# Kernel optimization log

Hardware: AMD Instinct MI355X
Metric: run time of the kernel (lower is better)

## Reference

```python
import jax, jax.numpy as jnp
import numpy as np

NDIM = 1024
NHEAD = 16
B, T = 4, 2048
EPS = 1e-05
GELU_C = np.sqrt(2.0 / np.pi).astype(np.float32)


def new_gelu(x):
    return 0.5 * x * (1.0 + jnp.tanh(GELU_C * (x + 0.044715 * x ** 3)))


def layer_norm(x, w, b):
    mu = jnp.mean(x, axis=-1, keepdims=True)
    var = jnp.var(x, axis=-1, keepdims=True)
    return (x - mu) * jax.lax.rsqrt(var + EPS) * w + b


def setup_inputs() -> dict:
    key = jax.random.key(0)
    ks = jax.random.split(key, 8)
    d, dff = NDIM, 4 * NDIM
    s = 0.02
    return {
        "x": jax.random.normal(ks[0], (B, T, d), jnp.float32),
        "ln1_w": jnp.ones((d,), jnp.float32),
        "ln1_b": jnp.zeros((d,), jnp.float32),
        "w_attn": jax.random.normal(ks[1], (d, 3 * d), jnp.float32) * s,
        "b_attn": jnp.zeros((3 * d,), jnp.float32),
        "w_proj": jax.random.normal(ks[2], (d, d), jnp.float32) * s,
        "b_proj": jnp.zeros((d,), jnp.float32),
        "ln2_w": jnp.ones((d,), jnp.float32),
        "ln2_b": jnp.zeros((d,), jnp.float32),
        "w_fc": jax.random.normal(ks[3], (d, dff), jnp.float32) * s,
        "b_fc": jnp.zeros((dff,), jnp.float32),
        "w_fc2": jax.random.normal(ks[4], (dff, d), jnp.float32) * s,
        "b_fc2": jnp.zeros((d,), jnp.float32),
    }


def reference(x, ln1_w, ln1_b, w_attn, b_attn, w_proj, b_proj,
              ln2_w, ln2_b, w_fc, b_fc, w_fc2, b_fc2):
    Bx, Tx, C = x.shape
    hd = C // NHEAD
    # --- attention ---
    h = layer_norm(x, ln1_w, ln1_b)
    qkv = h @ w_attn + b_attn                       # [B,T,3C]
    q, k, v = jnp.split(qkv, 3, axis=-1)
    q = q.reshape(Bx, Tx, NHEAD, hd).transpose(0, 2, 1, 3)  # [B,H,T,hd]
    k = k.reshape(Bx, Tx, NHEAD, hd).transpose(0, 2, 1, 3)
    v = v.reshape(Bx, Tx, NHEAD, hd).transpose(0, 2, 1, 3)
    att = jnp.einsum('bhqd,bhkd->bhqk', q, k) * (1.0 / np.sqrt(hd).astype(np.float32))
    causal = jnp.tril(jnp.ones((Tx, Tx), bool))
    att = jnp.where(causal[None, None], att, jnp.float32(-jnp.inf))
    att = jax.nn.softmax(att, axis=-1)
    y = jnp.einsum('bhqk,bhkd->bhqd', att, v)
    y = y.transpose(0, 2, 1, 3).reshape(Bx, Tx, C)
    x = x + y @ w_proj + b_proj
    # --- MLP ---
    h2 = layer_norm(x, ln2_w, ln2_b)
    x = x + new_gelu(h2 @ w_fc + b_fc) @ w_fc2 + b_fc2
    return x
```

## Files before the change

### kernel.cpp

```cpp
#include <hip/hip_runtime.h>

typedef __attribute__((ext_vector_type(8))) short short8;
typedef __attribute__((ext_vector_type(8))) unsigned short ushort8;
typedef __attribute__((ext_vector_type(4))) float f32x4;
typedef __attribute__((ext_vector_type(16))) float f32x16;
typedef __attribute__((ext_vector_type(2))) unsigned int uint2v;
typedef unsigned int uint32;

__device__ __forceinline__ unsigned short f2bf(float f){
  union { float f; unsigned int u; } x; x.f = f;
  unsigned int u = x.u;
  u += 0x7fffu + ((u >> 16) & 1u);
  return (unsigned short)(u >> 16);
}
__device__ __forceinline__ float bf2f(unsigned short s){
  union { float f; unsigned int u; } x; x.u = ((uint32)s) << 16; return x.f;
}

typedef __attribute__((address_space(1))) void gvoid;
typedef __attribute__((address_space(3))) void lvoid;
__device__ __forceinline__ void gload_lds16(const void* g, void* l){
  __builtin_amdgcn_global_load_lds((gvoid*)g, (lvoid*)l, 16, 0, 0);
}

__device__ __forceinline__ f32x4 mfma_bf16(short8 a, short8 b, f32x4 c){
  return __builtin_amdgcn_mfma_f32_16x16x32_bf16(a, b, c, 0, 0, 0);
}
__device__ __forceinline__ f32x16 mfma32(short8 a, short8 b, f32x16 c){
  return __builtin_amdgcn_mfma_f32_32x32x16_bf16(a, b, c, 0, 0, 0);
}

__device__ __forceinline__ uint32 cvtpk_bf(float lo, float hi){
  uint32 r;
  asm("v_cvt_pk_bf16_f32 %0, %1, %2" : "=v"(r) : "v"(lo), "v"(hi));
  return r;
}
__device__ __forceinline__ void plswap(uint32& a, uint32& b){
  auto r = __builtin_amdgcn_permlane32_swap(a, b, false, false);
  a = r[0]; b = r[1];
}

#if __has_builtin(__builtin_amdgcn_exp2f)
__device__ __forceinline__ float exp2g(float x){ return __builtin_amdgcn_exp2f(x); }
#else
__device__ __forceinline__ float exp2g(float x){ return exp2f(x); }
#endif
#if __has_builtin(__builtin_amdgcn_rcpf)
__device__ __forceinline__ float rcpg(float x){ return __builtin_amdgcn_rcpf(x); }
#else
__device__ __forceinline__ float rcpg(float x){ return 1.0f / x; }
#endif

__device__ __forceinline__ float gelu_fast(float v){
  const float u = 0.7978845608028654f * (v + 0.044715f * v * v * v);
  const float E = exp2g(2.8853900817779268f * u);
  return v - v * rcpg(1.0f + E);
}

__device__ __forceinline__ f32x16 zero16(){
  f32x16 z;
  #pragma unroll
  for (int i = 0; i < 16; i++) z[i] = 0.0f;
  return z;
}

__global__ __launch_bounds__(256) void wtrans_kernel(
    const float* __restrict__ w, unsigned short* __restrict__ wt, int K, int N)
{
  __shared__ float tile[32][33];
  const int n0 = blockIdx.x * 32;
  const int k0 = blockIdx.y * 32;
  const int t = threadIdx.x;
  #pragma unroll
  for (int i = 0; i < 4; i++){
    const int e = t + i * 256;
    const int r = e >> 5, c = e & 31;
    tile[r][c] = w[(size_t)(k0 + r) * N + n0 + c];
  }
  __syncthreads();
  #pragma unroll
  for (int i = 0; i < 4; i++){
    const int e = t + i * 256;
    const int r = e >> 5, c = e & 31;
    wt[(size_t)(n0 + r) * K + k0 + c] = f2bf(tile[c][r]);
  }
}

__global__ __launch_bounds__(256) void vtrans_kernel(
    const unsigned short* __restrict__ qkv, unsigned short* __restrict__ vt)
{
  __shared__ unsigned short tile[32][33];
  const int bh = blockIdx.z;
  const int b = bh >> 4, h = bh & 15;
  const int t0 = blockIdx.x * 32;
  const int f0 = blockIdx.y * 32;
  const int t = threadIdx.x;
  #pragma unroll
  for (int i = 0; i < 4; i++){
    const int e = t + i * 256;
    const int r = e >> 5, c = e & 31;
    tile[r][c] = qkv[(size_t)(b * 2048 + t0 + r) * 3072 + 2048 + h * 64 + f0 + c];
  }
  __syncthreads();
  #pragma unroll
  for (int i = 0; i < 4; i++){
    const int e = t + i * 256;
    const int r = e >> 5, c = e & 31;
    vt[((size_t)bh * 64 + f0 + r) * 2048 + t0 + c] = tile[c][r];
  }
}

__global__ __launch_bounds__(256) void ln_kernel(
    const float* __restrict__ x, const float* __restrict__ w, const float* __restrict__ b,
    unsigned short* __restrict__ out)
{
  const int row = blockIdx.x;
  const int t = threadIdx.x;
  const float4 v = ((const float4*)(x + (size_t)row * 1024))[t];
  float s  = v.x + v.y + v.z + v.w;
  float s2 = v.x * v.x + v.y * v.y + v.z * v.z + v.w * v.w;
  #pragma unroll
  for (int off = 32; off > 0; off >>= 1){
    s  += __shfl_xor(s, off);
    s2 += __shfl_xor(s2, off);
  }
  __shared__ float ps[8];
  const int wid = t >> 6;
  if ((t & 63) == 0){ ps[wid] = s; ps[4 + wid] = s2; }
  __syncthreads();
  s  = ps[0] + ps[1] + ps[2] + ps[3];
  s2 = ps[4] + ps[5] + ps[6] + ps[7];
  const float mu  = s * (1.0f / 1024.0f);
  const float var = s2 * (1.0f / 1024.0f) - mu * mu;
  const float rs  = rsqrtf(var + 1e-5f);
  const float4 wv = ((const float4*)w)[t];
  const float4 bv = ((const float4*)b)[t];
  ushort4 ov;
  ov.x = f2bf((v.x - mu) * rs * wv.x + bv.x);
  ov.y = f2bf((v.y - mu) * rs * wv.y + bv.y);
  ov.z = f2bf((v.z - mu) * rs * wv.z + bv.z);
  ov.w = f2bf((v.w - mu) * rs * wv.w + bv.w);
  ((ushort4*)(out + (size_t)row * 1024))[t] = ov;
}

#define EPI_BF16   0
#define EPI_RESF32 1
#define EPI_GELU   2

template<int EPI>
__global__ __launch_bounds__(256, 2) void gemm5_kernel(
    const unsigned short* __restrict__ A,
    const unsigned short* __restrict__ BT,
    const float* __restrict__ bias,
    const float* __restrict__ res,
    void* __restrict__ outp,
    int M, int N, int K)
{
  constexpr int SLOT = 24576;
  __shared__ __align__(16) char lds[3 * SLOT];

  const int nwg = gridDim.x;
  const int bid = blockIdx.x;
  const int wg = (bid & 7) * (nwg >> 3) + (bid >> 3);
  const int NT = N >> 8;
  const int mt = wg / NT;
  const int nti = wg - mt * NT;
  const int m0 = mt << 7;
  const int n0 = nti << 8;

  const int tid = threadIdx.x;
  const int lane = tid & 63;
  const int wid = tid >> 6;
  const int fr = lane & 15;
  const int fg = lane >> 4;

  const unsigned short* aSrc[2]; int aDst[2];
  #pragma unroll
  for (int l = 0; l < 2; l++){
    const int s = l * 256 + tid;
    const int r = s >> 2, c = s & 3;
    aSrc[l] = A + (size_t)(m0 + r) * K + ((c ^ ((r >> 1) & 3)) << 3);
    aDst[l] = s * 16;
  }
  const unsigned short* bSrc[4]; int bDst[4];
  #pragma unroll
  for (int l = 0; l < 4; l++){
    const int s = l * 256 + tid;
    const int r = s >> 2, c = s & 3;
    bSrc[l] = BT + (size_t)(n0 + r) * K + ((c ^ ((r >> 1) & 3)) << 3);
    bDst[l] = 8192 + s * 16;
  }

  int aOff[8], bOff[4];
  #pragma unroll
  for (int mi = 0; mi < 8; mi++){
    const int row = mi * 16 + fr;
    aOff[mi] = row * 64 + ((fg ^ ((row >> 1) & 3)) << 4);
  }
  #pragma unroll
  for (int nj = 0; nj < 4; nj++){
    const int row = wid * 64 + nj * 16 + fr;
    bOff[nj] = 8192 + row * 64 + ((fg ^ ((row >> 1) & 3)) << 4);
  }

  f32x4 acc[8][4];
  #pragma unroll
  for (int i = 0; i < 8; i++)
    #pragma unroll
    for (int j = 0; j < 4; j++) acc[i][j] = (f32x4){0.f, 0.f, 0.f, 0.f};

#define STAGE5(sl, slot) do { \
    gload_lds16(aSrc[0] + (size_t)(sl) * 32, lds + (slot) + aDst[0]); \
    gload_lds16(aSrc[1] + (size_t)(sl) * 32, lds + (slot) + aDst[1]); \
    gload_lds16(bSrc[0] + (size_t)(sl) * 32, lds + (slot) + bDst[0]); \
    gload_lds16(bSrc[1] + (size_t)(sl) * 32, lds + (slot) + bDst[1]); \
    gload_lds16(bSrc[2] + (size_t)(sl) * 32, lds + (slot) + bDst[2]); \
    gload_lds16(bSrc[3] + (size_t)(sl) * 32, lds + (slot) + bDst[3]); \
  } while (0)

  const int NS = K >> 5;

  STAGE5(0, 0);
  STAGE5(1, SLOT);
  asm volatile("s_waitcnt vmcnt(6)" ::: "memory");
  __builtin_amdgcn_s_barrier();
  asm volatile("" ::: "memory");

  int cs = 0, cg = 2 * SLOT;
  for (int s = 0; s < NS; s++){
    short8 aF[8], bF[4];
    #pragma unroll
    for (int mi = 0; mi < 8; mi++)
      aF[mi] = *(const short8*)(lds + cs + aOff[mi]);
    #pragma unroll
    for (int nj = 0; nj < 4; nj++)
      bF[nj] = *(const short8*)(lds + cs + bOff[nj]);
    if (s + 2 < NS) STAGE5(s + 2, cg);
    #pragma unroll
    for (int mi = 0; mi < 8; mi++)
      #pragma unroll
      for (int nj = 0; nj < 4; nj++)
        acc[mi][nj] = mfma_bf16(aF[mi], bF[nj], acc[mi][nj]);

    if (s + 2 < NS){
      asm volatile("s_waitcnt vmcnt(6)" ::: "memory");
    } else if (s + 1 < NS){
      asm volatile("s_waitcnt vmcnt(0)" ::: "memory");
    }
    __builtin_amdgcn_s_barrier();
    asm volatile("" ::: "memory");

    cs += SLOT; if (cs == 3 * SLOT) cs = 0;
    cg += SLOT; if (cg == 3 * SLOT) cg = 0;
  }
#undef STAGE5

  #pragma unroll
  for (int mi = 0; mi < 8; mi++){
    const int mrow = m0 + mi * 16 + fg * 4;
    #pragma unroll
    for (int nj = 0; nj < 4; nj++){
      const int ncol = n0 + wid * 64 + nj * 16 + fr;
      const float bv = bias[ncol];
      #pragma unroll
      for (int r2 = 0; r2 < 4; r2++){
        const size_t idx = (size_t)(mrow + r2) * N + ncol;
        float v = acc[mi][nj][r2] + bv;
        if (EPI == EPI_RESF32){
          ((float*)outp)[idx] = v + res[idx];
        } else if (EPI == EPI_GELU){
          ((unsigned short*)outp)[idx] = f2bf(gelu_fast(v));
        } else {
          ((unsigned short*)outp)[idx] = f2bf(v);
        }
      }
    }
  }
}

template<int EPI, int BN>
__global__ __launch_bounds__(512, 2) void gemm4_kernel(
    const unsigned short* __restrict__ A,
    const unsigned short* __restrict__ BT,
    const float* __restrict__ bias,
    const float* __restrict__ res,
    void* __restrict__ outp,
    int M, int N, int K)
{
  constexpr int MI   = (BN == 256) ? 8 : 4;
  constexpr int SP   = MI / 4;
  constexpr int NBL  = BN / 128;
  constexpr int WN   = (BN == 256) ? 4 : 2;
  constexpr int WROWS= (BN == 256) ? 128 : 64;
  constexpr int ASL  = 16384;
  constexpr int SLOT = ASL + BN * 64;
  __shared__ __align__(16) char lds[4 * SLOT];

  const int nwg = gridDim.x;
  const int bid = blockIdx.x;
  const int wg = (bid & 7) * (nwg >> 3) + (bid >> 3);
  const int NTile = N / BN;
  const int mt = wg / NTile;
  const int nti = wg - mt * NTile;
  const int m0 = mt << 8;
  const int n0 = nti * BN;

  const int tid = threadIdx.x;
  const int lane = tid & 63;
  const int wid = tid >> 6;
  const int wv_m = wid / WN;
  const int wv_n = wid % WN;
  const int fr = lane & 15;
  const int fg = lane >> 4;

  const unsigned short* aSrc[2];
  int aDst[2];
  #pragma unroll
  for (int l = 0; l < 2; l++){
    const int s = l * 512 + tid;
    const int r = s >> 2, c = s & 3;
    aSrc[l] = A + (size_t)(m0 + r) * K + ((c ^ ((r >> 1) & 3)) << 3);
    aDst[l] = s * 16;
  }
  const unsigned short* bSrc[NBL];
  int bDst[NBL];
  #pragma unroll
  for (int l = 0; l < NBL; l++){
    const int s = l * 512 + tid;
    const int r = s >> 2, c = s & 3;
    bSrc[l] = BT + (size_t)(n0 + r) * K + ((c ^ ((r >> 1) & 3)) << 3);
    bDst[l] = ASL + s * 16;
  }

  int aOff[MI], bOff[4];
  #pragma unroll
  for (int mi = 0; mi < MI; mi++){
    const int row = wv_m * WROWS + mi * 16 + fr;
    aOff[mi] = row * 64 + ((fg ^ ((row >> 1) & 3)) << 4);
  }
  #pragma unroll
  for (int nj = 0; nj < 4; nj++){
    const int row = wv_n * 64 + nj * 16 + fr;
    bOff[nj] = ASL + row * 64 + ((fg ^ ((row >> 1) & 3)) << 4);
  }

  f32x4 acc[MI][4];
  #pragma unroll
  for (int i = 0; i < MI; i++)
    #pragma unroll
    for (int j = 0; j < 4; j++) acc[i][j] = (f32x4){0.f, 0.f, 0.f, 0.f};

#define STAGE_A(sl, slot) do { \
    gload_lds16(aSrc[0] + (size_t)(sl) * 32, lds + (slot) + aDst[0]); \
    gload_lds16(aSrc[1] + (size_t)(sl) * 32, lds + (slot) + aDst[1]); \
  } while (0)
#define STAGE_B(sl, slot) do { \
    gload_lds16(bSrc[0] + (size_t)(sl) * 32, lds + (slot) + bDst[0]); \
    if (NBL == 2) gload_lds16(bSrc[1] + (size_t)(sl) * 32, lds + (slot) + bDst[1]); \
  } while (0)

  const int NS = K >> 5;

  STAGE_A(0, 0);        STAGE_B(0, 0);
  STAGE_A(1, SLOT);     STAGE_B(1, SLOT);
  STAGE_A(2, 2 * SLOT); STAGE_B(2, 2 * SLOT);
  if (BN == 256) asm volatile("s_waitcnt vmcnt(8)" ::: "memory");
  else           asm volatile("s_waitcnt vmcnt(6)" ::: "memory");
  __builtin_amdgcn_s_barrier();

  for (int s = 0; s < NS; s++){
    const int ss = (s & 3) * SLOT;
    const int sg = ((s + 3) & 3) * SLOT;
    const bool pf = (s + 3 < NS);
    short8 bF[4];
    #pragma unroll
    for (int sp = 0; sp < SP; sp++){
      short8 aF[4];
      #pragma unroll
      for (int i = 0; i < 4; i++)
        aF[i] = *(const short8*)(lds + ss + aOff[sp * 4 + i]);
      if (sp == 0){
        #pragma unroll
        for (int nj = 0; nj < 4; nj++)
          bF[nj] = *(const short8*)(lds + ss + bOff[nj]);
      }
      if (pf){
        if (SP == 2){
          if (sp == 0) STAGE_A(s + 3, sg);
          else         STAGE_B(s + 3, sg);
        } else {
          STAGE_A(s + 3, sg);
          STAGE_B(s + 3, sg);
        }
      }
      __builtin_amdgcn_s_barrier();
      asm volatile("s_waitcnt lgkmcnt(0)" ::: "memory");
      __builtin_amdgcn_sched_barrier(0);
      __builtin_amdgcn_s_setprio(1);
      #pragma unroll
      for (int i = 0; i < 4; i++)
        #pragma unroll
        for (int nj = 0; nj < 4; nj++)
          acc[sp * 4 + i][nj] = mfma_bf16(aF[i], bF[nj], acc[sp * 4 + i][nj]);
      __builtin_amdgcn_s_setprio(0);
      if (sp == SP - 1){
        if (s + 3 < NS){
          if (BN == 256) asm volatile("s_waitcnt vmcnt(8)" ::: "memory");
          else           asm volatile("s_waitcnt vmcnt(6)" ::: "memory");
        } else if (s + 2 < NS){
          if (BN == 256) asm volatile("s_waitcnt vmcnt(4)" ::: "memory");
          else           asm volatile("s_waitcnt vmcnt(3)" ::: "memory");
        } else if (s + 1 < NS){
          asm volatile("s_waitcnt vmcnt(0)" ::: "memory");
        }
      }
      __builtin_amdgcn_s_barrier();
    }
  }
#undef STAGE_A
#undef STAGE_B

  #pragma unroll
  for (int mi = 0; mi < MI; mi++){
    const int mrow = m0 + wv_m * WROWS + mi * 16 + fg * 4;
    #pragma unroll
    for (int nj = 0; nj < 4; nj++){
      const int ncol = n0 + wv_n * 64 + nj * 16 + fr;
      const float bv = bias[ncol];
      #pragma unroll
      for (int r2 = 0; r2 < 4; r2++){
        const size_t idx = (size_t)(mrow + r2) * N + ncol;
        float v = acc[mi][nj][r2] + bv;
        if (EPI == EPI_RESF32){
          ((float*)outp)[idx] = v + res[idx];
        } else if (EPI == EPI_GELU){
          ((unsigned short*)outp)[idx] = f2bf(gelu_fast(v));
        } else {
          ((unsigned short*)outp)[idx] = f2bf(v);
        }
      }
    }
  }
}

template<bool MASK>
__device__ __forceinline__ void attn_tile(
    const unsigned short* __restrict__ Kc, const unsigned short* __restrict__ Vc,
    const short8 (&qf)[4], int kvbase, int qg, int l31, int hi,
    float& m_r, float& lsum, f32x16& Oa, f32x16& Ob)
{
  f32x16 Sa = zero16();
  f32x16 Sb = zero16();
  const int xb = l31 & 7;
  #pragma unroll
  for (int kk = 0; kk < 4; kk++){
    const int x = kk * 2 + hi;
    const short8 k0 = *(const short8*)((const char*)Kc + l31 * 128 + ((x ^ xb) << 4));
    const short8 k1 = *(const short8*)((const char*)Kc + (l31 + 32) * 128 + ((x ^ xb) << 4));
    Sa = mfma32(k0, qf[kk], Sa);
    Sb = mfma32(k1, qf[kk], Sb);
  }
  if (MASK){
    #pragma unroll
    for (int r = 0; r < 16; r++){
      const int kva = kvbase + (r & 3) + 8 * (r >> 2) + 4 * hi;
      Sa[r] = (kva > qg)      ? -1e30f : Sa[r];
      Sb[r] = (kva + 32 > qg) ? -1e30f : Sb[r];
    }
  }
  float tmax = Sa[0];
  #pragma unroll
  for (int r = 1; r < 16; r++) tmax = fmaxf(tmax, Sa[r]);
  #pragma unroll
  for (int r = 0; r < 16; r++) tmax = fmaxf(tmax, Sb[r]);
  tmax = fmaxf(tmax, __shfl_xor(tmax, 32));
  if (__any(tmax > m_r + 10.0f)){
    const float mn = fmaxf(m_r, tmax);
    const float sc = exp2g(m_r - mn);
    m_r = mn;
    lsum *= sc;
    #pragma unroll
    for (int r = 0; r < 16; r++){ Oa[r] *= sc; Ob[r] *= sc; }
  }
  float rs = 0.0f;
  #pragma unroll
  for (int r = 0; r < 16; r++){
    Sa[r] = exp2g(Sa[r] - m_r); rs += Sa[r];
    Sb[r] = exp2g(Sb[r] - m_r); rs += Sb[r];
  }
  rs += __shfl_xor(rs, 32);
  lsum += rs;

  short8 pf[4];
  {
    uint32 a0 = cvtpk_bf(Sa[0], Sa[1]),   b0 = cvtpk_bf(Sa[4], Sa[5]);
    uint32 a1 = cvtpk_bf(Sa[2], Sa[3]),   b1 = cvtpk_bf(Sa[6], Sa[7]);
    plswap(a0, b0); plswap(a1, b1);
    uint32 a2 = cvtpk_bf(Sa[8], Sa[9]),   b2 = cvtpk_bf(Sa[12], Sa[13]);
    uint32 a3 = cvtpk_bf(Sa[10], Sa[11]), b3 = cvtpk_bf(Sa[14], Sa[15]);
    plswap(a2, b2); plswap(a3, b3);
    union { uint32 u[4]; short8 s; } m0, m1;
    m0.u[0] = a0; m0.u[1] = a1; m0.u[2] = b0; m0.u[3] = b1;
    m1.u[0] = a2; m1.u[1] = a3; m1.u[2] = b2; m1.u[3] = b3;
    pf[0] = m0.s; pf[1] = m1.s;
  }
  {
    uint32 a0 = cvtpk_bf(Sb[0], Sb[1]),   b0 = cvtpk_bf(Sb[4], Sb[5]);
    uint32 a1 = cvtpk_bf(Sb[2], Sb[3]),   b1 = cvtpk_bf(Sb[6], Sb[7]);
    plswap(a0, b0); plswap(a1, b1);
    uint32 a2 = cvtpk_bf(Sb[8], Sb[9]),   b2 = cvtpk_bf(Sb[12], Sb[13]);
    uint32 a3 = cvtpk_bf(Sb[10], Sb[11]), b3 = cvtpk_bf(Sb[14], Sb[15]);
    plswap(a2, b2); plswap(a3, b3);
    union { uint32 u[4]; short8 s; } m0, m1;
    m0.u[0] = a0; m0.u[1] = a1; m0.u[2] = b0; m0.u[3] = b1;
    m1.u[0] = a2; m1.u[1] = a3; m1.u[2] = b2; m1.u[3] = b3;
    pf[2] = m0.s; pf[3] = m1.s;
  }
  #pragma unroll
  for (int kk = 0; kk < 4; kk++){
    const int x = kk * 2 + hi;
    const short8 v0 = *(const short8*)((const char*)Vc + l31 * 128 + ((x ^ xb) << 4));
    const short8 v1 = *(const short8*)((const char*)Vc + (l31 + 32) * 128 + ((x ^ xb) << 4));
    Oa = mfma32(v0, pf[kk], Oa);
    Ob = mfma32(v1, pf[kk], Ob);
  }
}

__global__ __launch_bounds__(256) void attn_kernel(
    const unsigned short* __restrict__ qkv,
    const unsigned short* __restrict__ vt,
    unsigned short* __restrict__ y)
{
  __shared__ __align__(16) unsigned short Klds[2][4096];
  __shared__ __align__(16) unsigned short Vlds[2][4096];
  const int bid = blockIdx.x;
  const int bh = bid & 63;
  const int qb_i = bid >> 6;
  const int b = bh >> 4, h = bh & 15;
  const int qb0 = qb_i * 128;
  const int tid = threadIdx.x;
  const int w = tid >> 6;
  const int lane = tid & 63;
  const int l31 = lane & 31;
  const int hi = lane >> 5;

  const int qrow_g = b * 2048 + qb0 + w * 32 + l31;
  const unsigned short* qp = qkv + (size_t)qrow_g * 3072 + h * 64;
  short8 qf[4];
  #pragma unroll
  for (int kk = 0; kk < 4; kk++){
    short8 raw = *(const short8*)&qp[kk * 16 + hi * 8];
    #pragma unroll
    for (int j = 0; j < 8; j++)
      qf[kk][j] = (short)f2bf(bf2f((unsigned short)raw[j]) * 0.18033688011112042f);
  }

  const int sr = tid >> 3;
  const int ce = ((tid & 7) ^ (sr & 7)) * 8;
  const unsigned short* kb = qkv + (size_t)(b * 2048) * 3072 + 1024 + h * 64;
  const unsigned short* vb = vt + (size_t)bh * 64 * 2048;

  f32x16 Oa = zero16(), Ob = zero16();
  float m_r = -1e30f, lsum = 0.0f;
  const int qmin = qb0 + w * 32;
  const int qmax = qmin + 31;
  const int qg = qmin + l31;
  const int nkv = (qb0 >> 6) + 2;

#define STAGE(t, bb) do { \
    const size_t kro = (size_t)((t) * 64 + sr) * 3072; \
    gload_lds16(kb + kro + ce,                         (char*)&Klds[bb][0] + tid * 16); \
    gload_lds16(kb + kro + (size_t)32 * 3072 + ce,     (char*)&Klds[bb][0] + 4096 + tid * 16); \
    gload_lds16(vb + (size_t)sr * 2048 + (t) * 64 + ce,        (char*)&Vlds[bb][0] + tid * 16); \
    gload_lds16(vb + (size_t)(sr + 32) * 2048 + (t) * 64 + ce, (char*)&Vlds[bb][0] + 4096 + tid * 16); \
  } while (0)

  STAGE(0, 0);
  __syncthreads();
  int cur = 0;
  for (int kvt = 0; kvt < nkv; kvt++){
    if (kvt + 1 < nkv){
      if (cur) STAGE(kvt + 1, 0); else STAGE(kvt + 1, 1);
    }
    if (kvt * 64 <= qmax){
      if (kvt * 64 + 63 <= qmin)
        attn_tile<false>(Klds[cur], Vlds[cur], qf, kvt * 64, qg, l31, hi, m_r, lsum, Oa, Ob);
      else
        attn_tile<true >(Klds[cur], Vlds[cur], qf, kvt * 64, qg, l31, hi, m_r, lsum, Oa, Ob);
    }
    __syncthreads();
    cur ^= 1;
  }
#undef STAGE

  const float inv = 1.0f / lsum;
  unsigned short* yp = y + (size_t)qrow_g * 1024 + h * 64;
  #pragma unroll
  for (int c2 = 0; c2 < 4; c2++){
    uint2v da, db;
    da.x = cvtpk_bf(Oa[4 * c2 + 0] * inv, Oa[4 * c2 + 1] * inv);
    da.y = cvtpk_bf(Oa[4 * c2 + 2] * inv, Oa[4 * c2 + 3] * inv);
    *(uint2v*)&yp[8 * c2 + 4 * hi] = da;
    db.x = cvtpk_bf(Ob[4 * c2 + 0] * inv, Ob[4 * c2 + 1] * inv);
    db.y = cvtpk_bf(Ob[4 * c2 + 2] * inv, Ob[4 * c2 + 3] * inv);
    *(uint2v*)&yp[32 + 8 * c2 + 4 * hi] = db;
  }
}

extern "C" void kernel_launch(void* const* d_in, const int* in_sizes, int n_in,
                              void* d_out, int out_size, void* d_ws, size_t ws_size,
                              hipStream_t stream)
{
  const float* x      = (const float*)d_in[0];
  const float* ln1_w  = (const float*)d_in[1];
  const float* ln1_b  = (const float*)d_in[2];
  const float* w_attn = (const float*)d_in[3];
  const float* b_attn = (const float*)d_in[4];
  const float* w_proj = (const float*)d_in[5];
  const float* b_proj = (const float*)d_in[6];
  const float* ln2_w  = (const float*)d_in[7];
  const float* ln2_b  = (const float*)d_in[8];
  const float* w_fc   = (const float*)d_in[9];
  const float* b_fc   = (const float*)d_in[10];
  const float* w_fc2  = (const float*)d_in[11];
  const float* b_fc2  = (const float*)d_in[12];

  char* ws = (char*)d_ws;
  unsigned short* wbT_attn = (unsigned short*)(ws + 0);
  unsigned short* wbT_proj = (unsigned short*)(ws + 6291456);
  unsigned short* wbT_fc   = (unsigned short*)(ws + 8388608);
  unsigned short* wbT_fc2  = (unsigned short*)(ws + 16777216);
  unsigned short* h_bf     = (unsigned short*)(ws + 25165824);
  unsigned short* qkv_bf   = (unsigned short*)(ws + 41943040);
  unsigned short* vt_bf    = (unsigned short*)(ws + 92274688);
  unsigned short* g_bf     = (unsigned short*)(ws + 41943040);
  unsigned short* y_bf     = (unsigned short*)(ws + 109051904);
  float*          x1       = (float*)(ws + 125829120);
  float* outf = (float*)d_out;

  wtrans_kernel<<<dim3(3072/32, 1024/32), 256, 0, stream>>>(w_attn, wbT_attn, 1024, 3072);
  wtrans_kernel<<<dim3(1024/32, 1024/32), 256, 0, stream>>>(w_proj, wbT_proj, 1024, 1024);
  wtrans_kernel<<<dim3(4096/32, 1024/32), 256, 0, stream>>>(w_fc,   wbT_fc,   1024, 4096);
  wtrans_kernel<<<dim3(1024/32, 4096/32), 256, 0, stream>>>(w_fc2,  wbT_fc2,  4096, 1024);

  ln_kernel<<<8192, 256, 0, stream>>>(x, ln1_w, ln1_b, h_bf);
  gemm5_kernel<EPI_BF16><<<768, 256, 0, stream>>>(
      h_bf, wbT_attn, b_attn, nullptr, qkv_bf, 8192, 3072, 1024);
  vtrans_kernel<<<dim3(64, 2, 64), 256, 0, stream>>>(qkv_bf, vt_bf);
  attn_kernel<<<1024, 256, 0, stream>>>(qkv_bf, vt_bf, y_bf);
  gemm4_kernel<EPI_RESF32, 128><<<256, 512, 0, stream>>>(
      y_bf, wbT_proj, b_proj, x, x1, 8192, 1024, 1024);
  ln_kernel<<<8192, 256, 0, stream>>>(x1, ln2_w, ln2_b, h_bf);
  gemm5_kernel<EPI_GELU><<<1024, 256, 0, stream>>>(
      h_bf, wbT_fc, b_fc, nullptr, g_bf, 8192, 4096, 1024);
  gemm4_kernel<EPI_RESF32, 128><<<256, 512, 0, stream>>>(
      g_bf, wbT_fc2, b_fc2, x1, outf, 8192, 1024, 4096);
}
```

Measured before the change: 359.3 us.

## Replace N=1024 GEMMs with 64x256-tile, 2-wave kernel using 3-slot pipeline

Swaps the 512-thread 256x128-tile GEMM used for the attention projection and FC2 for a new 128-thread kernel with 64x256 tiles. Each of the two waves covers 64 rows by 128 columns, and the kernel uses a 3-slot LDS ring with prefetch distance 2 and one barrier per K step. The intent is to launch 512 smaller blocks so the 256 CUs are better filled, and to reduce barrier and sub-phase overhead. In exchange each block gets less A-operand reuse and fewer waves to hide latency, and the setprio and scheduling barriers are dropped.

```diff
diff --git a/kernel.cpp b/kernel.cpp
--- a/kernel.cpp
+++ b/kernel.cpp
@@ -278,8 +278,8 @@
   }
 }
 
-template<int EPI, int BN>
-__global__ __launch_bounds__(512, 2) void gemm4_kernel(
+template<int EPI>
+__global__ __launch_bounds__(128, 2) void gemm6_kernel(
     const unsigned short* __restrict__ A,
     const unsigned short* __restrict__ BT,
     const float* __restrict__ bias,
@@ -287,145 +287,115 @@
     void* __restrict__ outp,
     int M, int N, int K)
 {
-  constexpr int MI   = (BN == 256) ? 8 : 4;
-  constexpr int SP   = MI / 4;
-  constexpr int NBL  = BN / 128;
-  constexpr int WN   = (BN == 256) ? 4 : 2;
-  constexpr int WROWS= (BN == 256) ? 128 : 64;
-  constexpr int ASL  = 16384;
-  constexpr int SLOT = ASL + BN * 64;
-  __shared__ __align__(16) char lds[4 * SLOT];
+  constexpr int SLOT = 20480;
+  __shared__ __align__(16) char lds[3 * SLOT];
 
   const int nwg = gridDim.x;
   const int bid = blockIdx.x;
   const int wg = (bid & 7) * (nwg >> 3) + (bid >> 3);
-  const int NTile = N / BN;
-  const int mt = wg / NTile;
-  const int nti = wg - mt * NTile;
-  const int m0 = mt << 8;
-  const int n0 = nti * BN;
+  const int NT = N >> 8;
+  const int mt = wg / NT;
+  const int nti = wg - mt * NT;
+  const int m0 = mt << 6;
+  const int n0 = nti << 8;
 
   const int tid = threadIdx.x;
   const int lane = tid & 63;
   const int wid = tid >> 6;
-  const int wv_m = wid / WN;
-  const int wv_n = wid % WN;
   const int fr = lane & 15;
   const int fg = lane >> 4;
 
-  const unsigned short* aSrc[2];
-  int aDst[2];
+  const unsigned short* aSrc[2]; int aDst[2];
   #pragma unroll
   for (int l = 0; l < 2; l++){
-    const int s = l * 512 + tid;
+    const int s = l * 128 + tid;
     const int r = s >> 2, c = s & 3;
     aSrc[l] = A + (size_t)(m0 + r) * K + ((c ^ ((r >> 1) & 3)) << 3);
     aDst[l] = s * 16;
   }
-  const unsigned short* bSrc[NBL];
-  int bDst[NBL];
-  #pragma unroll
-  for (int l = 0; l < NBL; l++){
-    const int s = l * 512 + tid;
+  const unsigned short* bSrc[8]; int bDst[8];
+  #pragma unroll
+  for (int l = 0; l < 8; l++){
+    const int s = l * 128 + tid;
     const int r = s >> 2, c = s & 3;
     bSrc[l] = BT + (size_t)(n0 + r) * K + ((c ^ ((r >> 1) & 3)) << 3);
-    bDst[l] = ASL + s * 16;
-  }
-
-  int aOff[MI], bOff[4];
-  #pragma unroll
-  for (int mi = 0; mi < MI; mi++){
-    const int row = wv_m * WROWS + mi * 16 + fr;
+    bDst[l] = 4096 + s * 16;
+  }
+
+  int aOff[4], bOff[8];
+  #pragma unroll
+  for (int mi = 0; mi < 4; mi++){
+    const int row = mi * 16 + fr;
     aOff[mi] = row * 64 + ((fg ^ ((row >> 1) & 3)) << 4);
   }
   #pragma unroll
-  for (int nj = 0; nj < 4; nj++){
-    const int row = wv_n * 64 + nj * 16 + fr;
-    bOff[nj] = ASL + row * 64 + ((fg ^ ((row >> 1) & 3)) << 4);
-  }
-
-  f32x4 acc[MI][4];
-  #pragma unroll
-  for (int i = 0; i < MI; i++)
-    #pragma unroll
-    for (int j = 0; j < 4; j++) acc[i][j] = (f32x4){0.f, 0.f, 0.f, 0.f};
-
-#define STAGE_A(sl, slot) do { \
+  for (int nj = 0; nj < 8; nj++){
+    const int row = wid * 128 + nj * 16 + fr;
+    bOff[nj] = 4096 + row * 64 + ((fg ^ ((row >> 1) & 3)) << 4);
+  }
+
+  f32x4 acc[4][8];
+  #pragma unroll
+  for (int i = 0; i < 4; i++)
+    #pragma unroll
+    for (int j = 0; j < 8; j++) acc[i][j] = (f32x4){0.f, 0.f, 0.f, 0.f};
+
+#define STAGE6(sl, slot) do { \
     gload_lds16(aSrc[0] + (size_t)(sl) * 32, lds + (slot) + aDst[0]); \
     gload_lds16(aSrc[1] + (size_t)(sl) * 32, lds + (slot) + aDst[1]); \
+    gload_lds16(bSrc[0] + (size_t)(sl) * 32, lds + (slot) + bDst[0]); \
+    gload_lds16(bSrc[1] + (size_t)(sl) * 32, lds + (slot) + bDst[1]); \
+    gload_lds16(bSrc[2] + (size_t)(sl) * 32, lds + (slot) + bDst[2]); \
+    gload_lds16(bSrc[3] + (size_t)(sl) * 32, lds + (slot) + bDst[3]); \
+    gload_lds16(bSrc[4] + (size_t)(sl) * 32, lds + (slot) + bDst[4]); \
+    gload_lds16(bSrc[5] + (size_t)(sl) * 32, lds + (slot) + bDst[5]); \
+    gload_lds16(bSrc[6] + (size_t)(sl) * 32, lds + (slot) + bDst[6]); \
+    gload_lds16(bSrc[7] + (size_t)(sl) * 32, lds + (slot) + bDst[7]); \
   } while (0)
-#define STAGE_B(sl, slot) do { \
-    gload_lds16(bSrc[0] + (size_t)(sl) * 32, lds + (slot) + bDst[0]); \
-    if (NBL == 2) gload_lds16(bSrc[1] + (size_t)(sl) * 32, lds + (slot) + bDst[1]); \
-  } while (0)
 
   const int NS = K >> 5;
 
-  STAGE_A(0, 0);        STAGE_B(0, 0);
-  STAGE_A(1, SLOT);     STAGE_B(1, SLOT);
-  STAGE_A(2, 2 * SLOT); STAGE_B(2, 2 * SLOT);
-  if (BN == 256) asm volatile("s_waitcnt vmcnt(8)" ::: "memory");
-  else           asm volatile("s_waitcnt vmcnt(6)" ::: "memory");
+  STAGE6(0, 0);
+  STAGE6(1, SLOT);
+  asm volatile("s_waitcnt vmcnt(10)" ::: "memory");
   __builtin_amdgcn_s_barrier();
-
+  asm volatile("" ::: "memory");
+
+  int cs = 0, cg = 2 * SLOT;
   for (int s = 0; s < NS; s++){
-    const int ss = (s & 3) * SLOT;
-    const int sg = ((s + 3) & 3) * SLOT;
-    const bool pf = (s + 3 < NS);
-    short8 bF[4];
-    #pragma unroll
-    for (int sp = 0; sp < SP; sp++){
-      short8 aF[4];
+    short8 aF[4], bF[8];
+    #pragma unroll
+    for (int mi = 0; mi < 4; mi++)
+      aF[mi] = *(const short8*)(lds + cs + aOff[mi]);
+    #pragma unroll
+    for (int nj = 0; nj < 8; nj++)
+      bF[nj] = *(const short8*)(lds + cs + bOff[nj]);
+    if (s + 2 < NS) STAGE6(s + 2, cg);
+    #pragma unroll
+    for (int mi = 0; mi < 4; mi++)
       #pragma unroll
-      for (int i = 0; i < 4; i++)
-        aF[i] = *(const short8*)(lds + ss + aOff[sp * 4 + i]);
-      if (sp == 0){
-        #pragma unroll
-        for (int nj = 0; nj < 4; nj++)
-          bF[nj] = *(const short8*)(lds + ss + bOff[nj]);
-      }
-      if (pf){
-        if (SP == 2){
-          if (sp == 0) STAGE_A(s + 3, sg);
-          else         STAGE_B(s + 3, sg);
-        } else {
-          STAGE_A(s + 3, sg);
-          STAGE_B(s + 3, sg);
-        }
-      }
-      __builtin_amdgcn_s_barrier();
-      asm volatile("s_waitcnt lgkmcnt(0)" ::: "memory");
-      __builtin_amdgcn_sched_barrier(0);
-      __builtin_amdgcn_s_setprio(1);
-      #pragma unroll
-      for (int i = 0; i < 4; i++)
-        #pragma unroll
-        for (int nj = 0; nj < 4; nj++)
-          acc[sp * 4 + i][nj] = mfma_bf16(aF[i], bF[nj], acc[sp * 4 + i][nj]);
-      __builtin_amdgcn_s_setprio(0);
-      if (sp == SP - 1){
-        if (s + 3 < NS){
-          if (BN == 256) asm volatile("s_waitcnt vmcnt(8)" ::: "memory");
-          else           asm volatile("s_waitcnt vmcnt(6)" ::: "memory");
-        } else if (s + 2 < NS){
-          if (BN == 256) asm volatile("s_waitcnt vmcnt(4)" ::: "memory");
-          else           asm volatile("s_waitcnt vmcnt(3)" ::: "memory");
-        } else if (s + 1 < NS){
-          asm volatile("s_waitcnt vmcnt(0)" ::: "memory");
-        }
-      }
-      __builtin_amdgcn_s_barrier();
+      for (int nj = 0; nj < 8; nj++)
+        acc[mi][nj] = mfma_bf16(aF[mi], bF[nj], acc[mi][nj]);
+
+    if (s + 2 < NS){
+      asm volatile("s_waitcnt vmcnt(10)" ::: "memory");
+    } else if (s + 1 < NS){
+      asm volatile("s_waitcnt vmcnt(0)" ::: "memory");
     }
-  }
-#undef STAGE_A
-#undef STAGE_B
-
-  #pragma unroll
-  for (int mi = 0; mi < MI; mi++){
-    const int mrow = m0 + wv_m * WROWS + mi * 16 + fg * 4;
-    #pragma unroll
-    for (int nj = 0; nj < 4; nj++){
-      const int ncol = n0 + wv_n * 64 + nj * 16 + fr;
+    __builtin_amdgcn_s_barrier();
+    asm volatile("" ::: "memory");
+
+    cs += SLOT; if (cs == 3 * SLOT) cs = 0;
+    cg += SLOT; if (cg == 3 * SLOT) cg = 0;
+  }
+#undef STAGE6
+
+  #pragma unroll
+  for (int mi = 0; mi < 4; mi++){
+    const int mrow = m0 + mi * 16 + fg * 4;
+    #pragma unroll
+    for (int nj = 0; nj < 8; nj++){
+      const int ncol = n0 + wid * 128 + nj * 16 + fr;
       const float bv = bias[ncol];
       #pragma unroll
       for (int r2 = 0; r2 < 4; r2++){
@@ -648,11 +618,11 @@
       h_bf, wbT_attn, b_attn, nullptr, qkv_bf, 8192, 3072, 1024);
   vtrans_kernel<<<dim3(64, 2, 64), 256, 0, stream>>>(qkv_bf, vt_bf);
   attn_kernel<<<1024, 256, 0, stream>>>(qkv_bf, vt_bf, y_bf);
-  gemm4_kernel<EPI_RESF32, 128><<<256, 512, 0, stream>>>(
+  gemm6_kernel<EPI_RESF32><<<512, 128, 0, stream>>>(
       y_bf, wbT_proj, b_proj, x, x1, 8192, 1024, 1024);
   ln_kernel<<<8192, 256, 0, stream>>>(x1, ln2_w, ln2_b, h_bf);
   gemm5_kernel<EPI_GELU><<<1024, 256, 0, stream>>>(
       h_bf, wbT_fc, b_fc, nullptr, g_bf, 8192, 4096, 1024);
-  gemm4_kernel<EPI_RESF32, 128><<<256, 512, 0, stream>>>(
+  gemm6_kernel<EPI_RESF32><<<512, 128, 0, stream>>>(
       g_bf, wbT_fc2, b_fc2, x1, outf, 8192, 1024, 4096);
 }
```

Result: slower. 377.6 us (+5.1%).
